# Performance work log

Hardware: AMD Instinct MI355X
Metric: run time of the kernel (lower is better)

## Reference

```python
import jax, jax.numpy as jnp
import numpy as np

SR = 22050
N_FFT = 2048
HOP = 512
N_HARM = 5


def setup_inputs() -> dict:
    key = jax.random.key(0)
    audio = jax.random.normal(key, (32, 655360), dtype=jnp.float32)
    return {"audio": audio}


def _stft_mag(audio):
    """Matches torchaudio.transforms.Spectrogram(n_fft, hop, power=None, hann window):
    center=True with reflect padding, periodic Hann, onesided rfft. Returns |STFT|
    of shape (B, n_fft//2+1, T)."""
    pad = N_FFT // 2
    x = jnp.pad(audio, ((0, 0), (pad, pad)), mode="reflect")
    n_frames = 1 + audio.shape[1] // HOP
    # strided framing: (B, T, n_fft)
    idx = jnp.arange(n_frames)[:, None] * HOP + jnp.arange(N_FFT)[None, :]
    frames = x[:, idx]
    # periodic Hann window (torch.hann_window default)
    win = (0.5 * (1.0 - jnp.cos(2.0 * jnp.pi * jnp.arange(N_FFT) / N_FFT))).astype(jnp.float32)
    spec = jnp.fft.rfft(frames * win, axis=-1)  # (B, T, F)
    return jnp.abs(spec).transpose(0, 2, 1)     # (B, F, T)


def reference(audio):
    mag = _stft_mag(audio)                     # (B, F, T)
    B, F, T = mag.shape
    f0 = jnp.argmax(mag, axis=1)               # (B, T) int bin of peak per frame
    h = jnp.arange(1, N_HARM + 1)              # harmonics 1..H
    hbins = jnp.clip(f0[:, None, :] * h[None, :, None], 0, F - 1)  # (B, H, T)
    energy = jnp.take_along_axis(mag, hbins, axis=1)               # (B, H, T)
    return jnp.log10(energy + 1e-10)
```

## Files before the change

### kernel.cpp

```cpp
#include <hip/hip_runtime.h>
#include <math.h>

#define HOP 512
#define N_HARM 5
#define PI_D 3.14159265358979323846

#define P2(a) ((a) + ((a) >> 4))

__device__ __forceinline__ float2 cmul(float2 a, float2 b) {
    return make_float2(a.x * b.x - a.y * b.y, a.x * b.y + a.y * b.x);
}
__device__ __forceinline__ float2 cadd(float2 a, float2 b) {
    return make_float2(a.x + b.x, a.y + b.y);
}
__device__ __forceinline__ float2 csub(float2 a, float2 b) {
    return make_float2(a.x - b.x, a.y - b.y);
}

__global__ void hfe_setup_tables(float2* __restrict__ tw, float* __restrict__ win) {
    int i = blockIdx.x * blockDim.x + threadIdx.x;
    if (i < 1024) {
        double ang = -2.0 * PI_D * (double)i / 2048.0;
        tw[i] = make_float2((float)cos(ang), (float)sin(ang));
    }
    if (i < 2048) {
        double c = cos(2.0 * PI_D * (double)i / 2048.0);
        win[i] = (float)(0.5 * (1.0 - c));
    }
}

#define STAGE(S, D, LOG2M, SHIFT, LAST)                                        \
  {                                                                            \
    const int M_ = 1 << (LOG2M);                                               \
    const int j_ = tid >> (LOG2M);                                             \
    const int k_ = tid & (M_ - 1);                                             \
    const float2 va = S[P2(tid)];                                              \
    const float2 vb = S[P2(tid + 256)];                                        \
    const float2 vc = S[P2(tid + 512)];                                        \
    const float2 vd = S[P2(tid + 768)];                                        \
    const float2 t0 = cadd(va, vc);                                            \
    const float2 t1 = csub(va, vc);                                            \
    const float2 t2 = cadd(vb, vd);                                            \
    const float2 t3 = make_float2(vb.y - vd.y, -(vb.x - vd.x));   \
    const float2 u0 = cadd(t0, t2);                                            \
    const float2 u1 = cadd(t1, t3);                                            \
    const float2 u2 = csub(t0, t2);                                            \
    const float2 u3 = csub(t1, t3);                                            \
    const int ob = k_ + (j_ << ((LOG2M) + 2));                                 \
    if (LAST) {                                                                \
      D[P2(ob)]          = u0;                                                 \
      D[P2(ob + M_)]     = u1;                                                 \
      D[P2(ob + 2 * M_)] = u2;                                                 \
      D[P2(ob + 3 * M_)] = u3;                                                 \
    } else {                                                                   \
      const float2 w1 = tw[j_ << (SHIFT)];                                     \
      const float2 w2 = tw[j_ << ((SHIFT) + 1)];                               \
      const float2 w3 = cmul(w1, w2);                                          \
      D[P2(ob)]          = u0;                                                 \
      D[P2(ob + M_)]     = cmul(w1, u1);                                       \
      D[P2(ob + 2 * M_)] = cmul(w2, u2);                                       \
      D[P2(ob + 3 * M_)] = cmul(w3, u3);                                       \
    }                                                                          \
    __syncthreads();                                                           \
  }

__launch_bounds__(256)
__global__ void hfe_kernel(const float* __restrict__ audio,
                           const float2* __restrict__ tw,
                           const float* __restrict__ win,
                           float* __restrict__ out,
                           int L, int T) {
    __shared__ float2 A[1088], B[1088];
    __shared__ float wbest[4];
    __shared__ int   widx[4];
    __shared__ int   s_f0;
    float* mag = reinterpret_cast<float*>(A);

    const int tid   = threadIdx.x;
    const int frame = blockIdx.x;
    const int b     = frame / T;
    const int t     = frame - b * T;
    const long base = (long)b * (long)L;
    const int start = t * HOP - 1024;

    if (start >= 0 && start + 2048 <= L) {
        const float4* a4 = reinterpret_cast<const float4*>(audio + base + start);
        const float4* w4 = reinterpret_cast<const float4*>(win);
        #pragma unroll
        for (int p = 0; p < 2; ++p) {
            const int f = tid + p * 256;
            const float4 x = a4[f];
            const float4 w = w4[f];
            A[P2(2 * f)]     = make_float2(x.x * w.x, x.y * w.y);
            A[P2(2 * f + 1)] = make_float2(x.z * w.z, x.w * w.w);
        }
    } else {
        for (int n = tid; n < 1024; n += 256) {
            const int i0 = 2 * n, i1 = 2 * n + 1;
            int p0 = start + i0;
            p0 = (p0 < 0) ? -p0 : p0;
            p0 = (p0 >= L) ? (2 * L - 2 - p0) : p0;
            int p1 = start + i1;
            p1 = (p1 < 0) ? -p1 : p1;
            p1 = (p1 >= L) ? (2 * L - 2 - p1) : p1;
            A[P2(n)] = make_float2(audio[base + p0] * win[i0],
                                   audio[base + p1] * win[i1]);
        }
    }
    __syncthreads();

    STAGE(A, B, 0, 1, false)
    STAGE(B, A, 2, 3, false)
    STAGE(A, B, 4, 5, false)
    STAGE(B, A, 6, 7, false)
    STAGE(A, B, 8, 9, true)

    float best = -1.0f;
    int   bidx = 0;
    #pragma unroll
    for (int p = 0; p < 4; ++p) {
        const int k  = tid + p * 256;
        const int km = (1024 - k) & 1023;
        const float2 zk = B[P2(k)];
        const float2 zm = B[P2(km)];
        const float zer = 0.5f * (zk.x + zm.x), zei = 0.5f * (zk.y - zm.y);
        const float zor = 0.5f * (zk.y + zm.y), zoi = 0.5f * (zm.x - zk.x);
        const float2 w = tw[k];
        const float xr = zer + (w.x * zor - w.y * zoi);
        const float xi = zei + (w.x * zoi + w.y * zor);
        const float m2 = xr * xr + xi * xi;
        mag[k] = m2;
        if (m2 > best) { best = m2; bidx = k; }
        if (k == 0) {
            const float xn = zer - zor;
            const float m2n = xn * xn;
            mag[1024] = m2n;
            if (m2n > best) { best = m2n; bidx = 1024; }
        }
    }

    #pragma unroll
    for (int off = 32; off > 0; off >>= 1) {
        const float ov = __shfl_xor(best, off);
        const int   oi = __shfl_xor(bidx, off);
        if (ov > best || (ov == best && oi < bidx)) { best = ov; bidx = oi; }
    }
    const int wv = tid >> 6;
    if ((tid & 63) == 0) { wbest[wv] = best; widx[wv] = bidx; }
    __syncthreads();
    if (tid == 0) {
        float bb = wbest[0];
        int   bx = widx[0];
        #pragma unroll
        for (int w = 1; w < 4; ++w) {
            if (wbest[w] > bb || (wbest[w] == bb && widx[w] < bx)) {
                bb = wbest[w];
                bx = widx[w];
            }
        }
        s_f0 = bx;
    }
    __syncthreads();

    if (tid < N_HARM) {
        int bin = s_f0 * (tid + 1);
        if (bin > 1024) bin = 1024;
        const float e = sqrtf(mag[bin]);
        out[((long)b * N_HARM + tid) * (long)T + t] = log10f(e + 1e-10f);
    }
}

extern "C" void kernel_launch(void* const* d_in, const int* in_sizes, int n_in,
                              void* d_out, int out_size, void* d_ws, size_t ws_size,
                              hipStream_t stream) {
    const float* audio = (const float*)d_in[0];
    float*       out   = (float*)d_out;

    const int L = 655360;
    const int B = in_sizes[0] / L;
    const int T = 1 + L / HOP;

    float2* tw  = (float2*)d_ws;
    float*  win = (float*)((char*)d_ws + 1024 * sizeof(float2));

    hfe_setup_tables<<<8, 256, 0, stream>>>(tw, win);
    hfe_kernel<<<B * T, 256, 0, stream>>>(audio, tw, win, out, L, T);
}
```

Before: 227.7 us.

## Process one frame per wavefront with in-place register radix-4 FFT stages

Restructures the FFT so that each 64-lane wavefront handles one STFT frame, and two frames share a 128-thread block. Each lane holds 16 points in registers and runs in-place DIF radix-4 stages with float4 LDS accesses, and the last two stages are fused into one radix-16 step. The post-processing reads bins in digit-reversed order and computes the k and N-k bins together from one conjugate pair. The argmax is then reduced within the wavefront using shuffles only. This is meant to cut LDS traffic, the number of barriers and the cross-wave reduction, at the cost of more registers and a grid that assumes B*T is even.

```diff
diff --git a/kernel.cpp b/kernel.cpp
--- a/kernel.cpp
+++ b/kernel.cpp
@@ -5,79 +5,124 @@
 #define N_HARM 5
 #define PI_D 3.14159265358979323846
 
-#define P2(a) ((a) + ((a) >> 4))
-
+#define P2(a) ((a) + (((a) >> 4) << 1) + (((a) >> 6) << 1))
+
+__device__ __forceinline__ float2 cadd(float2 a, float2 b) { return make_float2(a.x + b.x, a.y + b.y); }
+__device__ __forceinline__ float2 csub(float2 a, float2 b) { return make_float2(a.x - b.x, a.y - b.y); }
 __device__ __forceinline__ float2 cmul(float2 a, float2 b) {
     return make_float2(a.x * b.x - a.y * b.y, a.x * b.y + a.y * b.x);
 }
-__device__ __forceinline__ float2 cadd(float2 a, float2 b) {
-    return make_float2(a.x + b.x, a.y + b.y);
-}
-__device__ __forceinline__ float2 csub(float2 a, float2 b) {
-    return make_float2(a.x - b.x, a.y - b.y);
-}
-
-__global__ void hfe_setup_tables(float2* __restrict__ tw, float* __restrict__ win) {
+
+__device__ __forceinline__ void bfly4(float2 a, float2 b, float2 c, float2 d,
+                                      float2& u0, float2& u1, float2& u2, float2& u3) {
+    const float2 t0 = cadd(a, c), t1 = csub(a, c), t2 = cadd(b, d);
+    const float2 t3 = make_float2(b.y - d.y, -(b.x - d.x));
+    u0 = cadd(t0, t2); u1 = cadd(t1, t3);
+    u2 = csub(t0, t2); u3 = csub(t1, t3);
+}
+
+__global__ void hfe_setup_tables(float2* __restrict__ tw2, float* __restrict__ win) {
     int i = blockIdx.x * blockDim.x + threadIdx.x;
-    if (i < 1024) {
+    if (i < 2048) {
         double ang = -2.0 * PI_D * (double)i / 2048.0;
-        tw[i] = make_float2((float)cos(ang), (float)sin(ang));
-    }
-    if (i < 2048) {
+        tw2[i] = make_float2((float)cos(ang), (float)sin(ang));
         double c = cos(2.0 * PI_D * (double)i / 2048.0);
         win[i] = (float)(0.5 * (1.0 - c));
     }
 }
 
-#define STAGE(S, D, LOG2M, SHIFT, LAST)                                        \
-  {                                                                            \
-    const int M_ = 1 << (LOG2M);                                               \
-    const int j_ = tid >> (LOG2M);                                             \
-    const int k_ = tid & (M_ - 1);                                             \
-    const float2 va = S[P2(tid)];                                              \
-    const float2 vb = S[P2(tid + 256)];                                        \
-    const float2 vc = S[P2(tid + 512)];                                        \
-    const float2 vd = S[P2(tid + 768)];                                        \
-    const float2 t0 = cadd(va, vc);                                            \
-    const float2 t1 = csub(va, vc);                                            \
-    const float2 t2 = cadd(vb, vd);                                            \
-    const float2 t3 = make_float2(vb.y - vd.y, -(vb.x - vd.x));   \
-    const float2 u0 = cadd(t0, t2);                                            \
-    const float2 u1 = cadd(t1, t3);                                            \
-    const float2 u2 = csub(t0, t2);                                            \
-    const float2 u3 = csub(t1, t3);                                            \
-    const int ob = k_ + (j_ << ((LOG2M) + 2));                                 \
-    if (LAST) {                                                                \
-      D[P2(ob)]          = u0;                                                 \
-      D[P2(ob + M_)]     = u1;                                                 \
-      D[P2(ob + 2 * M_)] = u2;                                                 \
-      D[P2(ob + 3 * M_)] = u3;                                                 \
-    } else {                                                                   \
-      const float2 w1 = tw[j_ << (SHIFT)];                                     \
-      const float2 w2 = tw[j_ << ((SHIFT) + 1)];                               \
-      const float2 w3 = cmul(w1, w2);                                          \
-      D[P2(ob)]          = u0;                                                 \
-      D[P2(ob + M_)]     = cmul(w1, u1);                                       \
-      D[P2(ob + 2 * M_)] = cmul(w2, u2);                                       \
-      D[P2(ob + 3 * M_)] = cmul(w3, u3);                                       \
-    }                                                                          \
-    __syncthreads();                                                           \
-  }
-
-__launch_bounds__(256)
+template<int LOG2S>
+__device__ __forceinline__ void dif_stage(float2* __restrict__ Z,
+                                          const float2* __restrict__ tw2,
+                                          const int lane) {
+    constexpr int S = 1 << LOG2S;
+    const int e0   = (4 * lane) & (S - 1);
+    const int blk  = (4 * lane) >> LOG2S;
+    const int base = (blk << (LOG2S + 2)) + e0;
+    float2 v[4][4];
+    #pragma unroll
+    for (int p = 0; p < 4; ++p) {
+        const float4* src = reinterpret_cast<const float4*>(&Z[P2(base + p * S)]);
+        const float4 lo = src[0], hi = src[1];
+        v[p][0] = make_float2(lo.x, lo.y); v[p][1] = make_float2(lo.z, lo.w);
+        v[p][2] = make_float2(hi.x, hi.y); v[p][3] = make_float2(hi.z, hi.w);
+    }
+    #pragma unroll
+    for (int i = 0; i < 4; ++i) {
+        float2 u0, u1, u2, u3;
+        bfly4(v[0][i], v[1][i], v[2][i], v[3][i], u0, u1, u2, u3);
+        const int x1 = (e0 + i) << (9 - LOG2S);
+        const float2 w1 = tw2[x1];
+        const float2 w2 = tw2[(2 * x1) & 2047];
+        const float2 w3 = tw2[(3 * x1) & 2047];
+        v[0][i] = u0;
+        v[1][i] = cmul(w1, u1);
+        v[2][i] = cmul(w2, u2);
+        v[3][i] = cmul(w3, u3);
+    }
+    #pragma unroll
+    for (int p = 0; p < 4; ++p) {
+        float4* dst = reinterpret_cast<float4*>(&Z[P2(base + p * S)]);
+        dst[0] = make_float4(v[p][0].x, v[p][0].y, v[p][1].x, v[p][1].y);
+        dst[1] = make_float4(v[p][2].x, v[p][2].y, v[p][3].x, v[p][3].y);
+    }
+}
+
+__device__ __forceinline__ void dif_stage41(float2* __restrict__ Z,
+                                            const float2* __restrict__ tw2,
+                                            const int lane) {
+    const int base = 16 * lane;
+    float2 r[16];
+    #pragma unroll
+    for (int c = 0; c < 4; ++c) {
+        const float4* src = reinterpret_cast<const float4*>(&Z[P2(base + 4 * c)]);
+        const float4 lo = src[0], hi = src[1];
+        r[4*c+0] = make_float2(lo.x, lo.y); r[4*c+1] = make_float2(lo.z, lo.w);
+        r[4*c+2] = make_float2(hi.x, hi.y); r[4*c+3] = make_float2(hi.z, hi.w);
+    }
+    #pragma unroll
+    for (int e = 0; e < 4; ++e) {
+        float2 u0, u1, u2, u3;
+        bfly4(r[e], r[e+4], r[e+8], r[e+12], u0, u1, u2, u3);
+        const float2 w1 = tw2[128 * e];
+        const float2 w2 = tw2[256 * e];
+        const float2 w3 = tw2[384 * e];
+        r[e]    = u0;
+        r[e+4]  = cmul(w1, u1);
+        r[e+8]  = cmul(w2, u2);
+        r[e+12] = cmul(w3, u3);
+    }
+    #pragma unroll
+    for (int b2 = 0; b2 < 4; ++b2) {
+        float2 u0, u1, u2, u3;
+        bfly4(r[4*b2], r[4*b2+1], r[4*b2+2], r[4*b2+3], u0, u1, u2, u3);
+        r[4*b2] = u0; r[4*b2+1] = u1; r[4*b2+2] = u2; r[4*b2+3] = u3;
+    }
+    #pragma unroll
+    for (int c = 0; c < 4; ++c) {
+        float4* dst = reinterpret_cast<float4*>(&Z[P2(base + 4 * c)]);
+        dst[0] = make_float4(r[4*c+0].x, r[4*c+0].y, r[4*c+1].x, r[4*c+1].y);
+        dst[1] = make_float4(r[4*c+2].x, r[4*c+2].y, r[4*c+3].x, r[4*c+3].y);
+    }
+}
+
+__device__ __forceinline__ int dr_hi(int lane6) {
+    return ((lane6 & 3) << 8) | (((lane6 >> 2) & 3) << 6) | (((lane6 >> 4) & 3) << 4);
+}
+
+__launch_bounds__(128)
 __global__ void hfe_kernel(const float* __restrict__ audio,
-                           const float2* __restrict__ tw,
+                           const float2* __restrict__ tw2,
                            const float* __restrict__ win,
                            float* __restrict__ out,
                            int L, int T) {
-    __shared__ float2 A[1088], B[1088];
-    __shared__ float wbest[4];
-    __shared__ int   widx[4];
-    __shared__ int   s_f0;
-    float* mag = reinterpret_cast<float*>(A);
-
-    const int tid   = threadIdx.x;
-    const int frame = blockIdx.x;
+    __shared__ float2 Zb[2][1184];
+    const int lane = threadIdx.x & 63;
+    const int fr   = threadIdx.x >> 6;
+    float2* Z  = Zb[fr];
+    float* mag = reinterpret_cast<float*>(Z);
+
+    const int frame = blockIdx.x * 2 + fr;
     const int b     = frame / T;
     const int t     = frame - b * T;
     const long base = (long)b * (long)L;
@@ -87,15 +132,17 @@
         const float4* a4 = reinterpret_cast<const float4*>(audio + base + start);
         const float4* w4 = reinterpret_cast<const float4*>(win);
         #pragma unroll
-        for (int p = 0; p < 2; ++p) {
-            const int f = tid + p * 256;
-            const float4 x = a4[f];
-            const float4 w = w4[f];
-            A[P2(2 * f)]     = make_float2(x.x * w.x, x.y * w.y);
-            A[P2(2 * f + 1)] = make_float2(x.z * w.z, x.w * w.w);
+        for (int c = 0; c < 8; ++c) {
+            const int q = lane * 8 + c;
+            const float4 x = a4[q];
+            const float4 w = w4[q];
+            float4* dst = reinterpret_cast<float4*>(&Z[P2(2 * q)]);
+            *dst = make_float4(x.x * w.x, x.y * w.y, x.z * w.z, x.w * w.w);
         }
     } else {
-        for (int n = tid; n < 1024; n += 256) {
+        #pragma unroll 4
+        for (int j = 0; j < 16; ++j) {
+            const int n = 16 * lane + j;
             const int i0 = 2 * n, i1 = 2 * n + 1;
             int p0 = start + i0;
             p0 = (p0 < 0) ? -p0 : p0;
@@ -103,40 +150,54 @@
             int p1 = start + i1;
             p1 = (p1 < 0) ? -p1 : p1;
             p1 = (p1 >= L) ? (2 * L - 2 - p1) : p1;
-            A[P2(n)] = make_float2(audio[base + p0] * win[i0],
+            Z[P2(n)] = make_float2(audio[base + p0] * win[i0],
                                    audio[base + p1] * win[i1]);
         }
     }
     __syncthreads();
 
-    STAGE(A, B, 0, 1, false)
-    STAGE(B, A, 2, 3, false)
-    STAGE(A, B, 4, 5, false)
-    STAGE(B, A, 6, 7, false)
-    STAGE(A, B, 8, 9, true)
-
+    dif_stage<8>(Z, tw2, lane);  __syncthreads();
+    dif_stage<6>(Z, tw2, lane);  __syncthreads();
+    dif_stage<4>(Z, tw2, lane);  __syncthreads();
+    dif_stage41(Z, tw2, lane);   __syncthreads();
+
+    const int DRH  = dr_hi(lane);
+    const int ln2  = (64 - lane) & 63;
+    const int DRH2 = dr_hi(ln2);
+    const bool l0  = (lane == 0);
+
+    float m2a[8], m2b[8];
     float best = -1.0f;
     int   bidx = 0;
     #pragma unroll
-    for (int p = 0; p < 4; ++p) {
-        const int k  = tid + p * 256;
-        const int km = (1024 - k) & 1023;
-        const float2 zk = B[P2(k)];
-        const float2 zm = B[P2(km)];
+    for (int j = 0; j < 8; ++j) {
+        const int k   = lane + 64 * j;
+        const int drl  = ((j & 3) << 2) | (j >> 2);
+        const int ja   = 15 - j;
+        const int jb   = (16 - j) & 15;
+        const int drla = ((ja & 3) << 2) | (ja >> 2);
+        const int drlb = ((jb & 3) << 2) | (jb >> 2);
+        const float2 zk = Z[P2(DRH | drl)];
+        const float2 zm = Z[P2(DRH2 | (l0 ? drlb : drla))];
         const float zer = 0.5f * (zk.x + zm.x), zei = 0.5f * (zk.y - zm.y);
         const float zor = 0.5f * (zk.y + zm.y), zoi = 0.5f * (zm.x - zk.x);
-        const float2 w = tw[k];
-        const float xr = zer + (w.x * zor - w.y * zoi);
-        const float xi = zei + (w.x * zoi + w.y * zor);
-        const float m2 = xr * xr + xi * xi;
-        mag[k] = m2;
-        if (m2 > best) { best = m2; bidx = k; }
-        if (k == 0) {
-            const float xn = zer - zor;
-            const float m2n = xn * xn;
-            mag[1024] = m2n;
-            if (m2n > best) { best = m2n; bidx = 1024; }
-        }
+        const float2 w  = tw2[k];
+        const float wr = w.x * zor - w.y * zoi;
+        const float wi = w.x * zoi + w.y * zor;
+        const float xpr = zer + wr, xpi = zei + wi;
+        const float xmr = zer - wr, xmi = zei - wi;
+        const float mp = xpr * xpr + xpi * xpi;
+        const float mm = xmr * xmr + xmi * xmi;
+        m2a[j] = mp; m2b[j] = mm;
+        const int kb = 1024 - k;
+        if (mp > best || (mp == best && k  < bidx)) { best = mp; bidx = k;  }
+        if (mm > best || (mm == best && kb < bidx)) { best = mm; bidx = kb; }
+    }
+    float m512 = 0.0f;
+    if (l0) {
+        const float2 z5 = Z[P2(2)];
+        m512 = z5.x * z5.x + z5.y * z5.y;
+        if (m512 > best || (m512 == best && 512 < bidx)) { best = m512; bidx = 512; }
     }
 
     #pragma unroll
@@ -145,28 +206,21 @@
         const int   oi = __shfl_xor(bidx, off);
         if (ov > best || (ov == best && oi < bidx)) { best = ov; bidx = oi; }
     }
-    const int wv = tid >> 6;
-    if ((tid & 63) == 0) { wbest[wv] = best; widx[wv] = bidx; }
+
     __syncthreads();
-    if (tid == 0) {
-        float bb = wbest[0];
-        int   bx = widx[0];
-        #pragma unroll
-        for (int w = 1; w < 4; ++w) {
-            if (wbest[w] > bb || (wbest[w] == bb && widx[w] < bx)) {
-                bb = wbest[w];
-                bx = widx[w];
-            }
-        }
-        s_f0 = bx;
-    }
+    #pragma unroll
+    for (int j = 0; j < 8; ++j) {
+        mag[lane + 64 * j]        = m2a[j];
+        mag[1024 - lane - 64 * j] = m2b[j];
+    }
+    if (l0) mag[512] = m512;
     __syncthreads();
 
-    if (tid < N_HARM) {
-        int bin = s_f0 * (tid + 1);
+    if (lane < N_HARM) {
+        int bin = bidx * (lane + 1);
         if (bin > 1024) bin = 1024;
         const float e = sqrtf(mag[bin]);
-        out[((long)b * N_HARM + tid) * (long)T + t] = log10f(e + 1e-10f);
+        out[((long)b * N_HARM + lane) * (long)T + t] = log10f(e + 1e-10f);
     }
 }
 
@@ -180,9 +234,9 @@
     const int B = in_sizes[0] / L;
     const int T = 1 + L / HOP;
 
-    float2* tw  = (float2*)d_ws;
-    float*  win = (float*)((char*)d_ws + 1024 * sizeof(float2));
-
-    hfe_setup_tables<<<8, 256, 0, stream>>>(tw, win);
-    hfe_kernel<<<B * T, 256, 0, stream>>>(audio, tw, win, out, L, T);
-}
+    float2* tw2 = (float2*)d_ws;
+    float*  win = (float*)((char*)d_ws + 2048 * sizeof(float2));
+
+    hfe_setup_tables<<<8, 256, 0, stream>>>(tw2, win);
+    hfe_kernel<<<(B * T) / 2, 128, 0, stream>>>(audio, tw2, win, out, L, T);
+}
```

Result: slower. 333.3 us (+46.4%).
